# Optimization experiments

Hardware: AMD Instinct MI355X
Metric: run time of the kernel (lower is better)

Reference implementation:

```python
import jax, jax.numpy as jnp
import numpy as np

B, D_IN, HID, DIM, M = 4096, 128, 200, 256, 32
SIGMA, OMEGA = 1.0, 1.7
LB, UB = 0.0, 1.0


def setup_inputs() -> dict:
    key = jax.random.key(0)
    ks = jax.random.split(key, 9)
    s = lambda d: 1.0 / jnp.sqrt(jnp.float32(d))
    return {
        "x": jax.random.normal(ks[0], (B, D_IN), jnp.float32),
        "b": jax.random.uniform(ks[1], (B, M), jnp.float32),
        "W1": jax.random.normal(ks[2], (D_IN, HID), jnp.float32) * s(D_IN),
        "b1": jnp.zeros((HID,), jnp.float32),
        "W2": jax.random.normal(ks[3], (HID, HID), jnp.float32) * s(HID),
        "b2": jnp.zeros((HID,), jnp.float32),
        "W3": jax.random.normal(ks[4], (HID, DIM), jnp.float32) * s(HID),
        "b3": jnp.zeros((DIM,), jnp.float32),
        "A": jax.random.normal(ks[5], (M, DIM), jnp.float32) * s(DIM),
        "step": 1000,
        "n_iter": 100,
    }


def reference(x, b, W1, b1, W2, b2, W3, b3, A, step, n_iter):
    # --- MLP: Dense(200) -> relu -> Dense(200) -> relu -> Dense(dim) ---
    h = jax.nn.relu(x @ W1 + b1)
    h = jax.nn.relu(h @ W2 + b2)
    y = h @ W3 + b3  # [B, DIM]

    # schedule = linear_schedule(0.0, 0.0, ...) -> alpha == 0.0 always
    alpha = jnp.float32(0.0)

    # --- projection onto {z : A z = b, LB <= z <= UB} via relaxed
    # Douglas-Rachford / SOR fixed-point iteration (sigma/omega) ---
    AAt_inv = jnp.linalg.inv(A @ A.T + 1e-6 * jnp.eye(M, dtype=A.dtype))

    def p_aff(z):  # affine equality projection, z: [B, DIM]
        r = z @ A.T - b            # [B, M] residual
        return z - (r @ AAt_inv) @ A

    def p_box(z):
        return jnp.clip(z, LB, UB)

    def body(z, _):
        u = p_aff(z)
        v = p_box(2.0 * u - z)     # reflection then box projection
        z = z + SIGMA * OMEGA * (v - u)
        return z, None

    z0 = y  # project.get_init(x): initialize fixed point at MLP output
    z_final, _ = jax.lax.scan(body, z0, None, length=n_iter)
    proj = p_aff(z_final)

    # interpolation between raw MLP output and projection (alpha == 0)
    out = alpha * y + (1.0 - alpha) * proj
    return out
```

## Files before the change

kernel.cpp:

```cpp
#include <hip/hip_runtime.h>
#include <hip/hip_bf16.h>

typedef float    f4v    __attribute__((ext_vector_type(4)));
typedef short    short8 __attribute__((ext_vector_type(8)));
typedef unsigned u2v    __attribute__((ext_vector_type(2)));

constexpr int Bn = 4096, TR = 16;

__device__ inline unsigned cvt2(float x, float y) {
  union { __hip_bfloat162 h; unsigned u; } c;
  c.h = __float22bfloat162_rn(float2{x, y});
  return c.u;
}
__device__ inline void split_pair(float x, float y, unsigned& hp, unsigned& lp) {
  hp = cvt2(x, y);
  float hx = __uint_as_float(hp << 16);
  float hy = __uint_as_float(hp & 0xffff0000u);
  lp = cvt2(x - hx, y - hy);
}
union S8U { unsigned u[4]; short8 s; };
__device__ inline void split8(const float v[8], short8& hi, short8& lo) {
  S8U h, l;
  #pragma unroll
  for (int d = 0; d < 4; ++d) split_pair(v[2 * d], v[2 * d + 1], h.u[d], l.u[d]);
  hi = h.s; lo = l.s;
}
__device__ inline void split8p(const float* p, short8& hi, short8& lo) {
  f4v a = *(const f4v*)p, b = *(const f4v*)(p + 4);
  float v[8] = {a[0], a[1], a[2], a[3], b[0], b[1], b[2], b[3]};
  split8(v, hi, lo);
}
__device__ inline f4v mfma16(short8 a, short8 b, f4v c) {
  return __builtin_amdgcn_mfma_f32_16x16x32_bf16(a, b, c, 0, 0, 0);
}
__device__ __attribute__((always_inline)) inline f4v gdot8(
    const short8 (&ah)[8], const short8 (&al)[8],
    const short8 (&bh)[8], const short8 (&bl)[8]) {
  f4v c = {0.f, 0.f, 0.f, 0.f};
  #pragma unroll
  for (int s = 0; s < 8; ++s) {
    c = mfma16(ah[s], bh[s], c);
    c = mfma16(al[s], bh[s], c);
    c = mfma16(ah[s], bl[s], c);
  }
  return c;
}

__global__ __launch_bounds__(256) void k_prep(const float* __restrict__ A,
                                              float* __restrict__ KAT) {
  __shared__ __align__(16) float As[32 * 256];
  __shared__ float Gm[32 * 68];
  __shared__ float GinvL[32 * 32];

  const int t = threadIdx.x;
  const int lane = t & 63, wv = t >> 6, quad = lane >> 4, l15 = lane & 15;
  const int T = wv & 1, kh = wv >> 1;

  for (int i = t; i < 2048; i += 256)
    ((f4v*)As)[i] = ((const f4v*)A)[i];
  __syncthreads();

  {
    short8 afh[2][8], afl[2][8];
    #pragma unroll
    for (int tt = 0; tt < 2; ++tt)
      #pragma unroll
      for (int s = 0; s < 8; ++s)
        split8p(As + (l15 + 16 * tt) * 256 + 32 * s + 8 * quad,
                afh[tt][s], afl[tt][s]);
    f4v cg;
    if      (wv == 0) cg = gdot8(afh[0], afl[0], afh[0], afl[0]);
    else if (wv == 1) cg = gdot8(afh[1], afl[1], afh[0], afl[0]);
    else if (wv == 2) cg = gdot8(afh[0], afl[0], afh[1], afl[1]);
    else              cg = gdot8(afh[1], afl[1], afh[1], afl[1]);
    #pragma unroll
    for (int r = 0; r < 4; ++r) {
      int gi = 16 * T + 4 * quad + r, gj = 16 * kh + l15;
      Gm[gi * 68 + gj]      = cg[r] + (gi == gj ? 1e-6f : 0.f);
      Gm[gi * 68 + 32 + gj] = (gi == gj) ? 1.f : 0.f;
    }
  }
  __syncthreads();

  if (wv == 0) {
    float gcol[32];
    #pragma unroll
    for (int i = 0; i < 32; ++i) gcol[i] = Gm[i * 68 + lane];
    #pragma unroll
    for (int k = 0; k < 32; ++k) {
      float ckk  = __shfl(gcol[k], k);
      float ipiv = 1.f / ckk;
      float pivj = gcol[k] * ipiv;
      gcol[k] = pivj;
      #pragma unroll
      for (int i = 0; i < 32; ++i) {
        if (i == k) continue;
        float cki = __shfl(gcol[i], k);
        gcol[i] = fmaf(-cki, pivj, gcol[i]);
      }
    }
    if (lane >= 32) {
      #pragma unroll
      for (int i = 0; i < 32; ++i) GinvL[i * 32 + (lane - 32)] = gcol[i];
    }
  }
  __syncthreads();

  {
    float res[32];
    #pragma unroll
    for (int m = 0; m < 32; ++m) res[m] = 0.f;
    for (int p = 0; p < 32; ++p) {
      float av = As[p * 256 + t];
      #pragma unroll
      for (int m4 = 0; m4 < 8; ++m4) {
        f4v g = *(const f4v*)&GinvL[p * 32 + 4 * m4];
        res[4 * m4 + 0] = fmaf(av, g[0], res[4 * m4 + 0]);
        res[4 * m4 + 1] = fmaf(av, g[1], res[4 * m4 + 1]);
        res[4 * m4 + 2] = fmaf(av, g[2], res[4 * m4 + 2]);
        res[4 * m4 + 3] = fmaf(av, g[3], res[4 * m4 + 3]);
      }
    }
    #pragma unroll
    for (int m4 = 0; m4 < 8; ++m4) {
      f4v v = {res[4 * m4], res[4 * m4 + 1], res[4 * m4 + 2], res[4 * m4 + 3]};
      *(f4v*)&KAT[t * 32 + 4 * m4] = v;
    }
  }
}

__global__ __launch_bounds__(512, 1) void k_main(
    const float* __restrict__ x,  const float* __restrict__ bmat,
    const float* __restrict__ W1, const float* __restrict__ b1,
    const float* __restrict__ W2, const float* __restrict__ b2,
    const float* __restrict__ W3, const float* __restrict__ b3,
    const float* __restrict__ A,  const float* __restrict__ KAT,
    const int* __restrict__ n_iter_p, float* __restrict__ out) {

  __shared__ __align__(16) float    ubuf[8768];
  __shared__ __align__(16) unsigned zfrag[4096];
  __shared__ __align__(16) unsigned rfrag[512];

  const int t = threadIdx.x;
  const int lane = t & 63, wv = t >> 6, quad = lane >> 4, l15 = lane & 15;
  const int row0 = blockIdx.x * TR;

  float* xs = ubuf;
  float* h1 = ubuf + 2112;
  float* h2 = ubuf + 5440;
  float* ys = ubuf;

  if (t < 512) {
    int r = t >> 5, c4 = t & 31;
    *(f4v*)&xs[r * 132 + 4 * c4] = *(const f4v*)&x[(size_t)(row0 + r) * 128 + 4 * c4];
  }
  __syncthreads();

  {
    const int rg = wv, oc = lane;
    const bool g3 = (oc < 8);
    float acc[4][2];

    #pragma unroll
    for (int oi = 0; oi < 4; ++oi) { acc[oi][0] = 0.f; acc[oi][1] = 0.f; }
    for (int k4 = 0; k4 < 32; ++k4) {
      f4v xv0 = *(const f4v*)&xs[(2 * rg + 0) * 132 + 4 * k4];
      f4v xv1 = *(const f4v*)&xs[(2 * rg + 1) * 132 + 4 * k4];
      #pragma unroll
      for (int kk = 0; kk < 4; ++kk) {
        const float* wr = W1 + (4 * k4 + kk) * 200 + oc;
        float w0 = wr[0], w1c = wr[64], w2c = wr[128];
        float w3c = g3 ? wr[192] : 0.f;
        acc[0][0] = fmaf(xv0[kk], w0, acc[0][0]);  acc[0][1] = fmaf(xv1[kk], w0, acc[0][1]);
        acc[1][0] = fmaf(xv0[kk], w1c, acc[1][0]); acc[1][1] = fmaf(xv1[kk], w1c, acc[1][1]);
        acc[2][0] = fmaf(xv0[kk], w2c, acc[2][0]); acc[2][1] = fmaf(xv1[kk], w2c, acc[2][1]);
        acc[3][0] = fmaf(xv0[kk], w3c, acc[3][0]); acc[3][1] = fmaf(xv1[kk], w3c, acc[3][1]);
      }
    }
    #pragma unroll
    for (int oi = 0; oi < 4; ++oi) {
      if (oi == 3 && !g3) continue;
      float bb = b1[oc + 64 * oi];
      h1[(2 * rg + 0) * 208 + oc + 64 * oi] = fmaxf(acc[oi][0] + bb, 0.f);
      h1[(2 * rg + 1) * 208 + oc + 64 * oi] = fmaxf(acc[oi][1] + bb, 0.f);
    }
    __syncthreads();

    #pragma unroll
    for (int oi = 0; oi < 4; ++oi) { acc[oi][0] = 0.f; acc[oi][1] = 0.f; }
    for (int k4 = 0; k4 < 50; ++k4) {
      f4v xv0 = *(const f4v*)&h1[(2 * rg + 0) * 208 + 4 * k4];
      f4v xv1 = *(const f4v*)&h1[(2 * rg + 1) * 208 + 4 * k4];
      #pragma unroll
      for (int kk = 0; kk < 4; ++kk) {
        const float* wr = W2 + (4 * k4 + kk) * 200 + oc;
        float w0 = wr[0], w1c = wr[64], w2c = wr[128];
        float w3c = g3 ? wr[192] : 0.f;
        acc[0][0] = fmaf(xv0[kk], w0, acc[0][0]);  acc[0][1] = fmaf(xv1[kk], w0, acc[0][1]);
        acc[1][0] = fmaf(xv0[kk], w1c, acc[1][0]); acc[1][1] = fmaf(xv1[kk], w1c, acc[1][1]);
        acc[2][0] = fmaf(xv0[kk], w2c, acc[2][0]); acc[2][1] = fmaf(xv1[kk], w2c, acc[2][1]);
        acc[3][0] = fmaf(xv0[kk], w3c, acc[3][0]); acc[3][1] = fmaf(xv1[kk], w3c, acc[3][1]);
      }
    }
    #pragma unroll
    for (int oi = 0; oi < 4; ++oi) {
      if (oi == 3 && !g3) continue;
      float bb = b2[oc + 64 * oi];
      h2[(2 * rg + 0) * 208 + oc + 64 * oi] = fmaxf(acc[oi][0] + bb, 0.f);
      h2[(2 * rg + 1) * 208 + oc + 64 * oi] = fmaxf(acc[oi][1] + bb, 0.f);
    }
    __syncthreads();

    #pragma unroll
    for (int oi = 0; oi < 4; ++oi) { acc[oi][0] = 0.f; acc[oi][1] = 0.f; }
    for (int k4 = 0; k4 < 50; ++k4) {
      f4v xv0 = *(const f4v*)&h2[(2 * rg + 0) * 208 + 4 * k4];
      f4v xv1 = *(const f4v*)&h2[(2 * rg + 1) * 208 + 4 * k4];
      #pragma unroll
      for (int kk = 0; kk < 4; ++kk) {
        const float* wr = W3 + (4 * k4 + kk) * 256 + oc;
        float w0 = wr[0], w1c = wr[64], w2c = wr[128], w3c = wr[192];
        acc[0][0] = fmaf(xv0[kk], w0, acc[0][0]);  acc[0][1] = fmaf(xv1[kk], w0, acc[0][1]);
        acc[1][0] = fmaf(xv0[kk], w1c, acc[1][0]); acc[1][1] = fmaf(xv1[kk], w1c, acc[1][1]);
        acc[2][0] = fmaf(xv0[kk], w2c, acc[2][0]); acc[2][1] = fmaf(xv1[kk], w2c, acc[2][1]);
        acc[3][0] = fmaf(xv0[kk], w3c, acc[3][0]); acc[3][1] = fmaf(xv1[kk], w3c, acc[3][1]);
      }
    }
    __syncthreads();
    #pragma unroll
    for (int oi = 0; oi < 4; ++oi) {
      float bb = b3[oc + 64 * oi];
      ys[(2 * rg + 0) * 260 + oc + 64 * oi] = acc[oi][0] + bb;
      ys[(2 * rg + 1) * 260 + oc + 64 * oi] = acc[oi][1] + bb;
    }
  }
  __syncthreads();

  const int T = wv;
  short8 aah[8], aal[8];
  f4v binit = {0.f, 0.f, 0.f, 0.f};
  if (wv < 2) {
    #pragma unroll
    for (int s = 0; s < 8; ++s) {
      const float* ap = A + (size_t)(l15 + 16 * T) * 256 + 32 * s + 8 * quad;
      float v[8];
      #pragma unroll
      for (int j = 0; j < 8; ++j) v[j] = ap[j];
      split8(v, aah[s], aal[s]);
    }
    f4v bv = *(const f4v*)&bmat[(size_t)(row0 + l15) * 32 + 16 * T + 4 * quad];
    binit = -bv;
  }

  short8 kanh[2], kanl[2];
  #pragma unroll
  for (int u = 0; u < 2; ++u) {
    const int U = 2 * wv + u;
    const float* kp = KAT + (size_t)(16 * U + l15) * 32 + 8 * quad;
    float v[8];
    #pragma unroll
    for (int j = 0; j < 8; ++j) v[j] = kp[j];
    split8(v, kanh[u], kanl[u]);
  }

  int zoff[2];
  #pragma unroll
  for (int u = 0; u < 2; ++u) {
    const int U = 2 * wv + u;
    const int qp = 2 * (U & 1) + (quad >> 1);
    zoff[u] = (((U >> 3) * 4 + ((U >> 1) & 3)) * 2) * 256
              + qp * 64 + l15 * 4 + 2 * (quad & 1);
  }

  float zr[2][4];
  #pragma unroll
  for (int u = 0; u < 2; ++u) {
    const int U = 2 * wv + u;
    f4v yv = *(const f4v*)&ys[l15 * 260 + 16 * U + 4 * quad];
    #pragma unroll
    for (int r = 0; r < 4; ++r) zr[u][r] = yv[r];
    unsigned h0, l0, h1_, l1_;
    split_pair(zr[u][0], zr[u][1], h0, l0);
    split_pair(zr[u][2], zr[u][3], h1_, l1_);
    u2v hv; hv[0] = h0; hv[1] = h1_;
    u2v lv; lv[0] = l0; lv[1] = l1_;
    *(u2v*)&zfrag[zoff[u]] = hv;
    *(u2v*)&zfrag[zoff[u] + 256] = lv;
  }
  __syncthreads();

  const int niter = n_iter_p[0];

  for (int it = 0; it <= niter; ++it) {
    if (wv < 2) {
      short8 zfh[8], zfl[8];
      #pragma unroll
      for (int s = 0; s < 8; ++s) {
        zfh[s] = *(const short8*)&zfrag[(s * 2 + 0) * 256 + lane * 4];
        zfl[s] = *(const short8*)&zfrag[(s * 2 + 1) * 256 + lane * 4];
      }
      f4v c0 = binit;
      f4v c1 = {0.f, 0.f, 0.f, 0.f};
      f4v c2 = {0.f, 0.f, 0.f, 0.f};
      f4v c3 = {0.f, 0.f, 0.f, 0.f};
      #pragma unroll
      for (int s4 = 0; s4 < 2; ++s4) {
        int s = 4 * s4;
        c0 = mfma16(aah[s+0], zfh[s+0], c0);
        c1 = mfma16(aah[s+1], zfh[s+1], c1);
        c2 = mfma16(aah[s+2], zfh[s+2], c2);
        c3 = mfma16(aah[s+3], zfh[s+3], c3);
        c0 = mfma16(aal[s+0], zfh[s+0], c0);
        c1 = mfma16(aal[s+1], zfh[s+1], c1);
        c2 = mfma16(aal[s+2], zfh[s+2], c2);
        c3 = mfma16(aal[s+3], zfh[s+3], c3);
        c0 = mfma16(aah[s+0], zfl[s+0], c0);
        c1 = mfma16(aah[s+1], zfl[s+1], c1);
        c2 = mfma16(aah[s+2], zfl[s+2], c2);
        c3 = mfma16(aah[s+3], zfl[s+3], c3);
      }
      f4v rA = (c0 + c1) + (c2 + c3);
      unsigned h0, l0, h1_, l1_;
      split_pair(rA[0], rA[1], h0, l0);
      split_pair(rA[2], rA[3], h1_, l1_);
      const int rb = (2 * T + (quad >> 1)) * 64 + l15 * 4 + 2 * (quad & 1);
      u2v hv; hv[0] = h0; hv[1] = h1_;
      u2v lv; lv[0] = l0; lv[1] = l1_;
      *(u2v*)&rfrag[rb] = hv;
      *(u2v*)&rfrag[rb + 256] = lv;
    }
    __syncthreads();

    const short8 rh = *(const short8*)&rfrag[0 * 256 + lane * 4];
    const short8 rl = *(const short8*)&rfrag[1 * 256 + lane * 4];
    f4v cB[2];
    #pragma unroll
    for (int u = 0; u < 2; ++u) {
      f4v cc = {0.f, 0.f, 0.f, 0.f};
      cc = mfma16(kanh[u], rh, cc);
      cc = mfma16(kanl[u], rh, cc);
      cc = mfma16(kanh[u], rl, cc);
      cB[u] = cc;
    }

    if (it < niter) {
      #pragma unroll
      for (int u = 0; u < 2; ++u) {
        #pragma unroll
        for (int r = 0; r < 4; ++r) {
          float z = zr[u][r], wvv = cB[u][r];
          float vv = fminf(fmaxf(z - 2.f * wvv, 0.f), 1.f);
          zr[u][r] = fmaf(1.7f, vv - z + wvv, z);
        }
        unsigned h0, l0, h1_, l1_;
        split_pair(zr[u][0], zr[u][1], h0, l0);
        split_pair(zr[u][2], zr[u][3], h1_, l1_);
        u2v hv; hv[0] = h0; hv[1] = h1_;
        u2v lv; lv[0] = l0; lv[1] = l1_;
        *(u2v*)&zfrag[zoff[u]] = hv;
        *(u2v*)&zfrag[zoff[u] + 256] = lv;
      }
      __syncthreads();
    } else {
      #pragma unroll
      for (int u = 0; u < 2; ++u) {
        const int U = 2 * wv + u;
        f4v ov;
        #pragma unroll
        for (int r = 0; r < 4; ++r) ov[r] = zr[u][r] - cB[u][r];
        *(f4v*)&out[(size_t)(row0 + l15) * 256 + 16 * U + 4 * quad] = ov;
      }
    }
  }
}

extern "C" void kernel_launch(void* const* d_in, const int* in_sizes, int n_in,
                              void* d_out, int out_size, void* d_ws, size_t ws_size,
                              hipStream_t stream) {
  const float* x    = (const float*)d_in[0];
  const float* bmat = (const float*)d_in[1];
  const float* W1   = (const float*)d_in[2];
  const float* b1   = (const float*)d_in[3];
  const float* W2   = (const float*)d_in[4];
  const float* b2   = (const float*)d_in[5];
  const float* W3   = (const float*)d_in[6];
  const float* b3   = (const float*)d_in[7];
  const float* A    = (const float*)d_in[8];
  const int*  n_it  = (const int*)d_in[10];
  float* KAT = (float*)d_ws;
  float* out = (float*)d_out;

  hipLaunchKernelGGL(k_prep, dim3(1), dim3(256), 0, stream, A, KAT);
  hipLaunchKernelGGL(k_main, dim3(Bn / TR), dim3(512), 0, stream,
                     x, bmat, W1, b1, W2, b2, W3, b3, A, KAT, n_it, out);
}
```

Measured before the change: 221.0 us.

## Fold affine projection into precomputed 256x256 projector with double-buffered z

Precomputes N = I - A^T (AA^T)^-1 A and c = A^T (AA^T)^-1 b, so each iteration's affine projection becomes a single 256x256 matrix product plus bias. This replaces the two-stage residual-then-correction path, which used only two waves for the first stage and needed an extra barrier. The z fragment buffer is double-buffered so each iteration needs one barrier, and launch bounds now allow two blocks per CU. Each iteration does more MFMA work (256-wide K instead of two 32-wide stages), and every wave holds a large set of N fragments in registers.

```diff
diff --git a/kernel.cpp b/kernel.cpp
--- a/kernel.cpp
+++ b/kernel.cpp
@@ -46,21 +46,22 @@
   return c;
 }
 
-__global__ __launch_bounds__(256) void k_prep(const float* __restrict__ A,
-                                              float* __restrict__ KAT) {
-  __shared__ __align__(16) float As[32 * 256];
+__global__ __launch_bounds__(1024) void k_prep(const float* __restrict__ A,
+                                               float* __restrict__ KAT,
+                                               float* __restrict__ NT) {
+  __shared__ __align__(16) float As[8192];
   __shared__ float Gm[32 * 68];
-  __shared__ float GinvL[32 * 32];
+  __shared__ float GinvL[1024];
+  __shared__ __align__(16) float KATs[8192];
 
   const int t = threadIdx.x;
   const int lane = t & 63, wv = t >> 6, quad = lane >> 4, l15 = lane & 15;
-  const int T = wv & 1, kh = wv >> 1;
-
-  for (int i = t; i < 2048; i += 256)
-    ((f4v*)As)[i] = ((const f4v*)A)[i];
-  __syncthreads();
-
-  {
+
+  for (int i = t; i < 2048; i += 1024) ((f4v*)As)[i] = ((const f4v*)A)[i];
+  __syncthreads();
+
+  if (wv < 4) {
+    const int T = wv & 1, kh = wv >> 1;
     short8 afh[2][8], afl[2][8];
     #pragma unroll
     for (int tt = 0; tt < 2; ++tt)
@@ -106,7 +107,7 @@
   }
   __syncthreads();
 
-  {
+  if (t < 256) {
     float res[32];
     #pragma unroll
     for (int m = 0; m < 32; ++m) res[m] = 0.f;
@@ -124,22 +125,50 @@
     #pragma unroll
     for (int m4 = 0; m4 < 8; ++m4) {
       f4v v = {res[4 * m4], res[4 * m4 + 1], res[4 * m4 + 2], res[4 * m4 + 3]};
-      *(f4v*)&KAT[t * 32 + 4 * m4] = v;
-    }
-  }
-}
-
-__global__ __launch_bounds__(512, 1) void k_main(
+      *(f4v*)&KATs[t * 32 + 4 * m4] = v;
+      *(f4v*)&KAT[t * 32 + 4 * m4]  = v;
+    }
+  }
+  __syncthreads();
+
+  {
+    short8 kth, ktl;
+    {
+      float v[8];
+      #pragma unroll
+      for (int j = 0; j < 8; ++j) v[j] = KATs[(16 * wv + l15) * 32 + 8 * quad + j];
+      split8(v, kth, ktl);
+    }
+    for (int tj = 0; tj < 16; ++tj) {
+      float v[8];
+      #pragma unroll
+      for (int jj = 0; jj < 8; ++jj)
+        v[jj] = As[(8 * quad + jj) * 256 + 16 * tj + l15];
+      short8 bsh, bsl;
+      split8(v, bsh, bsl);
+      f4v cg = {0.f, 0.f, 0.f, 0.f};
+      cg = mfma16(kth, bsh, cg);
+      cg = mfma16(ktl, bsh, cg);
+      cg = mfma16(kth, bsl, cg);
+      #pragma unroll
+      for (int r = 0; r < 4; ++r) {
+        int n = 16 * wv + 4 * quad + r, col = 16 * tj + l15;
+        NT[(size_t)n * 256 + col] = (n == col ? 1.f : 0.f) - cg[r];
+      }
+    }
+  }
+}
+
+__global__ __launch_bounds__(512, 2) void k_main(
     const float* __restrict__ x,  const float* __restrict__ bmat,
     const float* __restrict__ W1, const float* __restrict__ b1,
     const float* __restrict__ W2, const float* __restrict__ b2,
     const float* __restrict__ W3, const float* __restrict__ b3,
-    const float* __restrict__ A,  const float* __restrict__ KAT,
+    const float* __restrict__ KAT, const float* __restrict__ NT,
     const int* __restrict__ n_iter_p, float* __restrict__ out) {
 
   __shared__ __align__(16) float    ubuf[8768];
-  __shared__ __align__(16) unsigned zfrag[4096];
-  __shared__ __align__(16) unsigned rfrag[512];
+  __shared__ __align__(16) unsigned zfrag[2][4096];
 
   const int t = threadIdx.x;
   const int lane = t & 63, wv = t >> 6, quad = lane >> 4, l15 = lane & 15;
@@ -150,7 +179,7 @@
   float* h2 = ubuf + 5440;
   float* ys = ubuf;
 
-  if (t < 512) {
+  {
     int r = t >> 5, c4 = t & 31;
     *(f4v*)&xs[r * 132 + 4 * c4] = *(const f4v*)&x[(size_t)(row0 + r) * 128 + 4 * c4];
   }
@@ -236,31 +265,47 @@
   }
   __syncthreads();
 
-  const int T = wv;
-  short8 aah[8], aal[8];
-  f4v binit = {0.f, 0.f, 0.f, 0.f};
-  if (wv < 2) {
-    #pragma unroll
-    for (int s = 0; s < 8; ++s) {
-      const float* ap = A + (size_t)(l15 + 16 * T) * 256 + 32 * s + 8 * quad;
+  f4v cvec[2];
+  {
+    short8 bfh, bfl;
+    {
       float v[8];
       #pragma unroll
-      for (int j = 0; j < 8; ++j) v[j] = ap[j];
-      split8(v, aah[s], aal[s]);
-    }
-    f4v bv = *(const f4v*)&bmat[(size_t)(row0 + l15) * 32 + 16 * T + 4 * quad];
-    binit = -bv;
-  }
-
-  short8 kanh[2], kanl[2];
+      for (int j = 0; j < 8; ++j)
+        v[j] = bmat[(size_t)(row0 + l15) * 32 + 8 * quad + j];
+      split8(v, bfh, bfl);
+    }
+    #pragma unroll
+    for (int u = 0; u < 2; ++u) {
+      const int U = 2 * wv + u;
+      short8 kh_, kl_;
+      {
+        float v[8];
+        #pragma unroll
+        for (int j = 0; j < 8; ++j)
+          v[j] = KAT[(size_t)(16 * U + l15) * 32 + 8 * quad + j];
+        split8(v, kh_, kl_);
+      }
+      f4v cc = {0.f, 0.f, 0.f, 0.f};
+      cc = mfma16(kh_, bfh, cc);
+      cc = mfma16(kl_, bfh, cc);
+      cc = mfma16(kh_, bfl, cc);
+      cvec[u] = cc;
+    }
+  }
+
+  short8 nth[2][8], ntl[2][8];
   #pragma unroll
   for (int u = 0; u < 2; ++u) {
     const int U = 2 * wv + u;
-    const float* kp = KAT + (size_t)(16 * U + l15) * 32 + 8 * quad;
-    float v[8];
-    #pragma unroll
-    for (int j = 0; j < 8; ++j) v[j] = kp[j];
-    split8(v, kanh[u], kanl[u]);
+    #pragma unroll
+    for (int s = 0; s < 8; ++s) {
+      float v[8];
+      #pragma unroll
+      for (int j = 0; j < 8; ++j)
+        v[j] = NT[(size_t)(16 * U + l15) * 256 + 32 * s + 8 * quad + j];
+      split8(v, nth[u][s], ntl[u][s]);
+    }
   }
 
   int zoff[2];
@@ -284,90 +329,60 @@
     split_pair(zr[u][2], zr[u][3], h1_, l1_);
     u2v hv; hv[0] = h0; hv[1] = h1_;
     u2v lv; lv[0] = l0; lv[1] = l1_;
-    *(u2v*)&zfrag[zoff[u]] = hv;
-    *(u2v*)&zfrag[zoff[u] + 256] = lv;
+    *(u2v*)&zfrag[0][zoff[u]] = hv;
+    *(u2v*)&zfrag[0][zoff[u] + 256] = lv;
   }
   __syncthreads();
 
   const int niter = n_iter_p[0];
+  int p = 0;
 
   for (int it = 0; it <= niter; ++it) {
-    if (wv < 2) {
-      short8 zfh[8], zfl[8];
-      #pragma unroll
-      for (int s = 0; s < 8; ++s) {
-        zfh[s] = *(const short8*)&zfrag[(s * 2 + 0) * 256 + lane * 4];
-        zfl[s] = *(const short8*)&zfrag[(s * 2 + 1) * 256 + lane * 4];
-      }
-      f4v c0 = binit;
-      f4v c1 = {0.f, 0.f, 0.f, 0.f};
-      f4v c2 = {0.f, 0.f, 0.f, 0.f};
-      f4v c3 = {0.f, 0.f, 0.f, 0.f};
-      #pragma unroll
-      for (int s4 = 0; s4 < 2; ++s4) {
-        int s = 4 * s4;
-        c0 = mfma16(aah[s+0], zfh[s+0], c0);
-        c1 = mfma16(aah[s+1], zfh[s+1], c1);
-        c2 = mfma16(aah[s+2], zfh[s+2], c2);
-        c3 = mfma16(aah[s+3], zfh[s+3], c3);
-        c0 = mfma16(aal[s+0], zfh[s+0], c0);
-        c1 = mfma16(aal[s+1], zfh[s+1], c1);
-        c2 = mfma16(aal[s+2], zfh[s+2], c2);
-        c3 = mfma16(aal[s+3], zfh[s+3], c3);
-        c0 = mfma16(aah[s+0], zfl[s+0], c0);
-        c1 = mfma16(aah[s+1], zfl[s+1], c1);
-        c2 = mfma16(aah[s+2], zfl[s+2], c2);
-        c3 = mfma16(aah[s+3], zfl[s+3], c3);
-      }
-      f4v rA = (c0 + c1) + (c2 + c3);
-      unsigned h0, l0, h1_, l1_;
-      split_pair(rA[0], rA[1], h0, l0);
-      split_pair(rA[2], rA[3], h1_, l1_);
-      const int rb = (2 * T + (quad >> 1)) * 64 + l15 * 4 + 2 * (quad & 1);
-      u2v hv; hv[0] = h0; hv[1] = h1_;
-      u2v lv; lv[0] = l0; lv[1] = l1_;
-      *(u2v*)&rfrag[rb] = hv;
-      *(u2v*)&rfrag[rb + 256] = lv;
-    }
-    __syncthreads();
-
-    const short8 rh = *(const short8*)&rfrag[0 * 256 + lane * 4];
-    const short8 rl = *(const short8*)&rfrag[1 * 256 + lane * 4];
-    f4v cB[2];
-    #pragma unroll
-    for (int u = 0; u < 2; ++u) {
-      f4v cc = {0.f, 0.f, 0.f, 0.f};
-      cc = mfma16(kanh[u], rh, cc);
-      cc = mfma16(kanl[u], rh, cc);
-      cc = mfma16(kanh[u], rl, cc);
-      cB[u] = cc;
+    const unsigned* zb = zfrag[p];
+    f4v a0[2], a1[2];
+    a0[0] = cvec[0]; a0[1] = cvec[1];
+    a1[0] = f4v{0.f, 0.f, 0.f, 0.f};
+    a1[1] = f4v{0.f, 0.f, 0.f, 0.f};
+    #pragma unroll
+    for (int s = 0; s < 8; ++s) {
+      short8 zh = *(const short8*)&zb[(2 * s + 0) * 256 + lane * 4];
+      short8 zl = *(const short8*)&zb[(2 * s + 1) * 256 + lane * 4];
+      #pragma unroll
+      for (int u = 0; u < 2; ++u) {
+        f4v acc = (s & 1) ? a1[u] : a0[u];
+        acc = mfma16(nth[u][s], zh, acc);
+        acc = mfma16(ntl[u][s], zh, acc);
+        acc = mfma16(nth[u][s], zl, acc);
+        if (s & 1) a1[u] = acc; else a0[u] = acc;
+      }
     }
 
     if (it < niter) {
+      unsigned* zw = zfrag[p ^ 1];
       #pragma unroll
       for (int u = 0; u < 2; ++u) {
+        f4v uu = a0[u] + a1[u];
         #pragma unroll
         for (int r = 0; r < 4; ++r) {
-          float z = zr[u][r], wvv = cB[u][r];
-          float vv = fminf(fmaxf(z - 2.f * wvv, 0.f), 1.f);
-          zr[u][r] = fmaf(1.7f, vv - z + wvv, z);
+          float z = zr[u][r], uv = uu[r];
+          float vv = fminf(fmaxf(2.f * uv - z, 0.f), 1.f);
+          zr[u][r] = fmaf(1.7f, vv - uv, z);
         }
         unsigned h0, l0, h1_, l1_;
         split_pair(zr[u][0], zr[u][1], h0, l0);
         split_pair(zr[u][2], zr[u][3], h1_, l1_);
         u2v hv; hv[0] = h0; hv[1] = h1_;
         u2v lv; lv[0] = l0; lv[1] = l1_;
-        *(u2v*)&zfrag[zoff[u]] = hv;
-        *(u2v*)&zfrag[zoff[u] + 256] = lv;
+        *(u2v*)&zw[zoff[u]] = hv;
+        *(u2v*)&zw[zoff[u] + 256] = lv;
       }
       __syncthreads();
+      p ^= 1;
     } else {
       #pragma unroll
       for (int u = 0; u < 2; ++u) {
         const int U = 2 * wv + u;
-        f4v ov;
-        #pragma unroll
-        for (int r = 0; r < 4; ++r) ov[r] = zr[u][r] - cB[u][r];
+        f4v ov = a0[u] + a1[u];
         *(f4v*)&out[(size_t)(row0 + l15) * 256 + 16 * U + 4 * quad] = ov;
       }
     }
@@ -388,9 +403,10 @@
   const float* A    = (const float*)d_in[8];
   const int*  n_it  = (const int*)d_in[10];
   float* KAT = (float*)d_ws;
+  float* NT  = (float*)d_ws + 8192;
   float* out = (float*)d_out;
 
-  hipLaunchKernelGGL(k_prep, dim3(1), dim3(256), 0, stream, A, KAT);
+  hipLaunchKernelGGL(k_prep, dim3(1), dim3(1024), 0, stream, A, KAT, NT);
   hipLaunchKernelGGL(k_main, dim3(Bn / TR), dim3(512), 0, stream,
-                     x, bmat, W1, b1, W2, b2, W3, b3, A, KAT, n_it, out);
-}
+                     x, bmat, W1, b1, W2, b2, W3, b3, KAT, NT, n_it, out);
+}
```

Result: slower. 267.5 us (+21.1%).

## Fuse Gram-inverse prep into main kernel, recomputing A·Ginv per block

Applied to the files above, without the earlier changes.

Removes the separate single-block prep kernel that built (A A^T)^-1 and K = A^T Ginv in workspace. Every block of the main kernel now redundantly loads A into shared memory, forms the Gram matrix with plain FMA, inverts it with the one-wave Gauss-Jordan, and computes its own K fragments directly into registers. This drops a kernel launch and the serial dependency on a one-block kernel. The cost is duplicated prep work in every one of the 256 blocks and possibly more register pressure.

```diff
diff --git a/kernel.cpp b/kernel.cpp
--- a/kernel.cpp
+++ b/kernel.cpp
@@ -33,52 +33,53 @@
 __device__ inline f4v mfma16(short8 a, short8 b, f4v c) {
   return __builtin_amdgcn_mfma_f32_16x16x32_bf16(a, b, c, 0, 0, 0);
 }
-__device__ __attribute__((always_inline)) inline f4v gdot8(
-    const short8 (&ah)[8], const short8 (&al)[8],
-    const short8 (&bh)[8], const short8 (&bl)[8]) {
-  f4v c = {0.f, 0.f, 0.f, 0.f};
-  #pragma unroll
-  for (int s = 0; s < 8; ++s) {
-    c = mfma16(ah[s], bh[s], c);
-    c = mfma16(al[s], bh[s], c);
-    c = mfma16(ah[s], bl[s], c);
-  }
-  return c;
-}
-
-__global__ __launch_bounds__(256) void k_prep(const float* __restrict__ A,
-                                              float* __restrict__ KAT) {
-  __shared__ __align__(16) float As[32 * 256];
-  __shared__ float Gm[32 * 68];
-  __shared__ float GinvL[32 * 32];
+
+__global__ __launch_bounds__(512, 1) void k_fused(
+    const float* __restrict__ x,  const float* __restrict__ bmat,
+    const float* __restrict__ W1, const float* __restrict__ b1,
+    const float* __restrict__ W2, const float* __restrict__ b2,
+    const float* __restrict__ W3, const float* __restrict__ b3,
+    const float* __restrict__ A,  const int* __restrict__ n_iter_p,
+    float* __restrict__ out) {
+
+  __shared__ __align__(16) float    ubuf[8768];
+  __shared__ __align__(16) unsigned zfrag[4096];
+  __shared__ __align__(16) unsigned rfrag[512];
 
   const int t = threadIdx.x;
   const int lane = t & 63, wv = t >> 6, quad = lane >> 4, l15 = lane & 15;
-  const int T = wv & 1, kh = wv >> 1;
-
-  for (int i = t; i < 2048; i += 256)
-    ((f4v*)As)[i] = ((const f4v*)A)[i];
-  __syncthreads();
-
-  {
-    short8 afh[2][8], afl[2][8];
-    #pragma unroll
-    for (int tt = 0; tt < 2; ++tt)
-      #pragma unroll
-      for (int s = 0; s < 8; ++s)
-        split8p(As + (l15 + 16 * tt) * 256 + 32 * s + 8 * quad,
-                afh[tt][s], afl[tt][s]);
-    f4v cg;
-    if      (wv == 0) cg = gdot8(afh[0], afl[0], afh[0], afl[0]);
-    else if (wv == 1) cg = gdot8(afh[1], afl[1], afh[0], afl[0]);
-    else if (wv == 2) cg = gdot8(afh[0], afl[0], afh[1], afl[1]);
-    else              cg = gdot8(afh[1], afl[1], afh[1], afl[1]);
-    #pragma unroll
-    for (int r = 0; r < 4; ++r) {
-      int gi = 16 * T + 4 * quad + r, gj = 16 * kh + l15;
-      Gm[gi * 68 + gj]      = cg[r] + (gi == gj ? 1e-6f : 0.f);
-      Gm[gi * 68 + 32 + gj] = (gi == gj) ? 1.f : 0.f;
-    }
+  const int row0 = blockIdx.x * TR;
+
+  float* Ald   = ubuf;
+  float* Gm    = (float*)zfrag;
+  float* GinvL = (float*)zfrag + 2240;
+
+  for (int i = t; i < 2048; i += 512)
+    ((f4v*)Ald)[i] = ((const f4v*)A)[i];
+  __syncthreads();
+
+  #pragma unroll
+  for (int e = 0; e < 2; ++e) {
+    const int idx = t + 512 * e, gi = idx >> 5, gj = idx & 31;
+    f4v acc = {0.f, 0.f, 0.f, 0.f};
+    const f4v* ai = (const f4v*)(Ald + gi * 256);
+    const f4v* aj = (const f4v*)(Ald + gj * 256);
+    for (int k = 0; k < 64; ++k) acc += ai[k] * aj[k];
+    float s = acc[0] + acc[1] + acc[2] + acc[3];
+    if (gi == gj) s += 1e-6f;
+    Gm[gi * 68 + gj] = s;
+    Gm[gi * 68 + 32 + gj] = (gi == gj) ? 1.f : 0.f;
+  }
+
+  const int T = wv;
+  short8 aah[8], aal[8];
+  f4v binit = {0.f, 0.f, 0.f, 0.f};
+  if (wv < 2) {
+    #pragma unroll
+    for (int s = 0; s < 8; ++s)
+      split8p(Ald + (l15 + 16 * T) * 256 + 32 * s + 8 * quad, aah[s], aal[s]);
+    f4v bv = *(const f4v*)&bmat[(size_t)(row0 + l15) * 32 + 16 * T + 4 * quad];
+    binit = -bv;
   }
   __syncthreads();
 
@@ -106,51 +107,32 @@
   }
   __syncthreads();
 
-  {
-    float res[32];
-    #pragma unroll
-    for (int m = 0; m < 32; ++m) res[m] = 0.f;
+  short8 kanh[2], kanl[2];
+  #pragma unroll
+  for (int u = 0; u < 2; ++u) {
+    const int n = 16 * (2 * wv + u) + l15;
+    float acc[8];
+    #pragma unroll
+    for (int j = 0; j < 8; ++j) acc[j] = 0.f;
     for (int p = 0; p < 32; ++p) {
-      float av = As[p * 256 + t];
-      #pragma unroll
-      for (int m4 = 0; m4 < 8; ++m4) {
-        f4v g = *(const f4v*)&GinvL[p * 32 + 4 * m4];
-        res[4 * m4 + 0] = fmaf(av, g[0], res[4 * m4 + 0]);
-        res[4 * m4 + 1] = fmaf(av, g[1], res[4 * m4 + 1]);
-        res[4 * m4 + 2] = fmaf(av, g[2], res[4 * m4 + 2]);
-        res[4 * m4 + 3] = fmaf(av, g[3], res[4 * m4 + 3]);
-      }
-    }
-    #pragma unroll
-    for (int m4 = 0; m4 < 8; ++m4) {
-      f4v v = {res[4 * m4], res[4 * m4 + 1], res[4 * m4 + 2], res[4 * m4 + 3]};
-      *(f4v*)&KAT[t * 32 + 4 * m4] = v;
-    }
-  }
-}
-
-__global__ __launch_bounds__(512, 1) void k_main(
-    const float* __restrict__ x,  const float* __restrict__ bmat,
-    const float* __restrict__ W1, const float* __restrict__ b1,
-    const float* __restrict__ W2, const float* __restrict__ b2,
-    const float* __restrict__ W3, const float* __restrict__ b3,
-    const float* __restrict__ A,  const float* __restrict__ KAT,
-    const int* __restrict__ n_iter_p, float* __restrict__ out) {
-
-  __shared__ __align__(16) float    ubuf[8768];
-  __shared__ __align__(16) unsigned zfrag[4096];
-  __shared__ __align__(16) unsigned rfrag[512];
-
-  const int t = threadIdx.x;
-  const int lane = t & 63, wv = t >> 6, quad = lane >> 4, l15 = lane & 15;
-  const int row0 = blockIdx.x * TR;
+      float av = Ald[p * 256 + n];
+      f4v g0 = *(const f4v*)&GinvL[p * 32 + 8 * quad];
+      f4v g1 = *(const f4v*)&GinvL[p * 32 + 8 * quad + 4];
+      acc[0] = fmaf(av, g0[0], acc[0]); acc[1] = fmaf(av, g0[1], acc[1]);
+      acc[2] = fmaf(av, g0[2], acc[2]); acc[3] = fmaf(av, g0[3], acc[3]);
+      acc[4] = fmaf(av, g1[0], acc[4]); acc[5] = fmaf(av, g1[1], acc[5]);
+      acc[6] = fmaf(av, g1[2], acc[6]); acc[7] = fmaf(av, g1[3], acc[7]);
+    }
+    split8(acc, kanh[u], kanl[u]);
+  }
+  __syncthreads();
 
   float* xs = ubuf;
   float* h1 = ubuf + 2112;
   float* h2 = ubuf + 5440;
   float* ys = ubuf;
 
-  if (t < 512) {
+  {
     int r = t >> 5, c4 = t & 31;
     *(f4v*)&xs[r * 132 + 4 * c4] = *(const f4v*)&x[(size_t)(row0 + r) * 128 + 4 * c4];
   }
@@ -235,33 +217,6 @@
     }
   }
   __syncthreads();
-
-  const int T = wv;
-  short8 aah[8], aal[8];
-  f4v binit = {0.f, 0.f, 0.f, 0.f};
-  if (wv < 2) {
-    #pragma unroll
-    for (int s = 0; s < 8; ++s) {
-      const float* ap = A + (size_t)(l15 + 16 * T) * 256 + 32 * s + 8 * quad;
-      float v[8];
-      #pragma unroll
-      for (int j = 0; j < 8; ++j) v[j] = ap[j];
-      split8(v, aah[s], aal[s]);
-    }
-    f4v bv = *(const f4v*)&bmat[(size_t)(row0 + l15) * 32 + 16 * T + 4 * quad];
-    binit = -bv;
-  }
-
-  short8 kanh[2], kanl[2];
-  #pragma unroll
-  for (int u = 0; u < 2; ++u) {
-    const int U = 2 * wv + u;
-    const float* kp = KAT + (size_t)(16 * U + l15) * 32 + 8 * quad;
-    float v[8];
-    #pragma unroll
-    for (int j = 0; j < 8; ++j) v[j] = kp[j];
-    split8(v, kanh[u], kanl[u]);
-  }
 
   int zoff[2];
   #pragma unroll
@@ -387,10 +342,8 @@
   const float* b3   = (const float*)d_in[7];
   const float* A    = (const float*)d_in[8];
   const int*  n_it  = (const int*)d_in[10];
-  float* KAT = (float*)d_ws;
   float* out = (float*)d_out;
 
-  hipLaunchKernelGGL(k_prep, dim3(1), dim3(256), 0, stream, A, KAT);
-  hipLaunchKernelGGL(k_main, dim3(Bn / TR), dim3(512), 0, stream,
-                     x, bmat, W1, b1, W2, b2, W3, b3, A, KAT, n_it, out);
-}
+  hipLaunchKernelGGL(k_fused, dim3(Bn / TR), dim3(512), 0, stream,
+                     x, bmat, W1, b1, W2, b2, W3, b3, A, n_it, out);
+}
```

Result: slower. 243.6 us (+10.2%).
